# Kernel optimization log

Hardware: AMD Instinct MI355X
Metric: run time of the kernel (lower is better)

## Reference

```python
import jax, jax.numpy as jnp
import numpy as np

B, T, D_IN = 4096, 1024, 2
EMD, CELL, D_OUT = 128, 128, 5


def setup_inputs() -> dict:
    key = jax.random.key(0)
    ks = jax.random.split(key, 9)
    s = lambda k, shape, fan: jax.random.normal(k, shape, jnp.float32) / np.sqrt(fan)
    return {
        "inputs": jax.random.normal(ks[0], (B, T, D_IN), jnp.float32),
        "We": s(ks[1], (EMD, D_IN), D_IN),
        "be": s(ks[2], (EMD,), D_IN),
        "W_ih": s(ks[3], (4 * CELL, EMD), EMD),
        "W_hh": s(ks[4], (4 * CELL, CELL), CELL),
        "b_ih": s(ks[5], (4 * CELL,), CELL),
        "b_hh": s(ks[6], (4 * CELL,), CELL),
        "Wo": s(ks[7], (D_OUT, CELL), CELL),
        "bo": s(ks[8], (D_OUT,), CELL),
    }


def reference(inputs, We, be, W_ih, W_hh, b_ih, b_hh, Wo, bo):
    """VanillaLSTM forward: per-step embed MLP -> LSTMCell -> output MLP.
    inputs: [B, T, D_IN]; returns (outputs [B, T, D_OUT], h [B,CELL], c [B,CELL])."""
    Bsz = inputs.shape[0]
    cell = W_hh.shape[1]

    def step(hc, x_t):
        h, c = hc
        # input embedding MLP (Linear + ReLU, batch_norm=False)
        e = jax.nn.relu(x_t @ We.T + be)                      # [B, EMD]
        # torch.nn.LSTMCell gate math
        gates = e @ W_ih.T + b_ih + h @ W_hh.T + b_hh         # [B, 4*CELL]
        i, f, g, o = jnp.split(gates, 4, axis=-1)
        i, f, o = jax.nn.sigmoid(i), jax.nn.sigmoid(f), jax.nn.sigmoid(o)
        g = jnp.tanh(g)
        c_new = f * c + i * g
        h_new = o * jnp.tanh(c_new)
        # output embedding (Linear, no activation)
        y = h_new @ Wo.T + bo                                 # [B, D_OUT]
        return (h_new, c_new), y

    h0 = jnp.zeros((Bsz, cell), inputs.dtype)
    c0 = jnp.zeros((Bsz, cell), inputs.dtype)
    xs = jnp.swapaxes(inputs, 0, 1)                           # [T, B, D_IN]
    (h, c), ys = jax.lax.scan(step, (h0, c0), xs)
    outputs = jnp.swapaxes(ys, 0, 1)                          # [B, T, D_OUT]
    return outputs, h, c
```

## Files before the change

kernel.cpp:

```cpp
#include <hip/hip_runtime.h>
#include <hip/hip_bf16.h>


#define B_TOT 4096
#define T_LEN 1024
#define D_INP 2
#define EMD   128
#define CELL  128
#define D_OUT 5

#define ROWS  16
#define WAVES 8
#define BLOCK (WAVES * 64)
#define LDH   136

typedef short s8v  __attribute__((ext_vector_type(8)));
typedef short s4v  __attribute__((ext_vector_type(4)));
typedef float f32x4 __attribute__((ext_vector_type(4)));

#define BAR() asm volatile("s_waitcnt lgkmcnt(0)\n\ts_barrier" ::: "memory")

#if __has_builtin(__builtin_amdgcn_exp2f)
#define EXP2F(x) __builtin_amdgcn_exp2f(x)
#else
#define EXP2F(x) exp2f(x)
#endif
#if __has_builtin(__builtin_amdgcn_rcpf)
#define RCPF(x) __builtin_amdgcn_rcpf(x)
#else
#define RCPF(x) (1.0f / (x))
#endif

__device__ __forceinline__ float bf2f(short s) {
    unsigned int u = ((unsigned int)(unsigned short)s) << 16;
    return __builtin_bit_cast(float, u);
}
__device__ __forceinline__ short f2bf(float f) {
    unsigned int u = __builtin_bit_cast(unsigned int, f);
    u += 0x7fffu + ((u >> 16) & 1u);
    return (short)(u >> 16);
}
__device__ __forceinline__ unsigned int pk_bf16(float a, float b) {
    unsigned int ua = __builtin_bit_cast(unsigned int, a);
    unsigned int ub = __builtin_bit_cast(unsigned int, b);
    return ((ua + 0x8000u) >> 16) | ((ub + 0x8000u) & 0xffff0000u);
}
__device__ __forceinline__ float sigm(float x) {
    return RCPF(1.0f + EXP2F(-1.44269504f * x));
}
__device__ __forceinline__ float tanh_fast(float x) {
    return 2.0f * RCPF(1.0f + EXP2F(-2.88539008f * x)) - 1.0f;
}
__device__ __forceinline__ s8v load8_f32_to_bf16(const float* p) {
    float4 a = *(const float4*)p;
    float4 b = *(const float4*)(p + 4);
    s8v r;
    r[0] = f2bf(a.x); r[1] = f2bf(a.y); r[2] = f2bf(a.z); r[3] = f2bf(a.w);
    r[4] = f2bf(b.x); r[5] = f2bf(b.y); r[6] = f2bf(b.z); r[7] = f2bf(b.w);
    return r;
}

__global__ __launch_bounds__(BLOCK, 1)
void lstm_persistent(const float* __restrict__ x,
                     const float* __restrict__ We,
                     const float* __restrict__ be,
                     const float* __restrict__ Wih,
                     const float* __restrict__ Whh,
                     const float* __restrict__ bih,
                     const float* __restrict__ bhh,
                     const float* __restrict__ Wo,
                     const float* __restrict__ bo,
                     float* __restrict__ out)
{
    __shared__ short h_lds[2][ROWS][LDH];
    __shared__ short e_lds[2][ROWS][LDH];

    const int tid  = threadIdx.x;
    const int lane = tid & 63;
    const int w    = tid >> 6;
    const int n16  = lane & 15;
    const int q    = lane >> 4;
    const int q8   = q * 8;
    const int b0   = blockIdx.x * ROWS;
    const int ch0  = w * 16 + q * 4;

    float* out_y = out;
    float* out_h = out + (size_t)B_TOT * T_LEN * D_OUT;
    float* out_c = out_h + (size_t)B_TOT * CELL;

    s8v wih_f[4][4], whh_f[4][4];
    #pragma unroll
    for (int g = 0; g < 4; ++g) {
        const int row = g * CELL + w * 16 + n16;
        #pragma unroll
        for (int kt = 0; kt < 4; ++kt) {
            wih_f[g][kt] = load8_f32_to_bf16(Wih + row * EMD  + kt * 32 + q8);
            whh_f[g][kt] = load8_f32_to_bf16(Whh + row * CELL + kt * 32 + q8);
        }
    }
    float4 bias4[4];
    #pragma unroll
    for (int g = 0; g < 4; ++g) {
        float4 bi = *(const float4*)(bih + g * CELL + ch0);
        float4 bh = *(const float4*)(bhh + g * CELL + ch0);
        bias4[g] = make_float4(bi.x + bh.x, bi.y + bh.y, bi.z + bh.z, bi.w + bh.w);
    }

    s8v wo_f[4];
    float bo_r[4];
    {
        s8v z = {0, 0, 0, 0, 0, 0, 0, 0};
        #pragma unroll
        for (int kt = 0; kt < 4; ++kt) wo_f[kt] = z;
        if (w == 0 && n16 < D_OUT) {
            #pragma unroll
            for (int kt = 0; kt < 4; ++kt)
                wo_f[kt] = load8_f32_to_bf16(Wo + n16 * CELL + kt * 32 + q8);
        }
        #pragma unroll
        for (int r = 0; r < 4; ++r) {
            const int oc = q * 4 + r;
            bo_r[r] = (w == 0 && oc < D_OUT) ? bo[oc] : 0.0f;
        }
    }

    const int er  = tid >> 5;
    const int jj0 = (tid & 31) * 4;
    float weA[4], weB[4], bev[4];
    #pragma unroll
    for (int jl = 0; jl < 4; ++jl) {
        weA[jl] = We[(jj0 + jl) * 2 + 0];
        weB[jl] = We[(jj0 + jl) * 2 + 1];
        bev[jl] = be[jj0 + jl];
    }
    const float* xrow = x + (size_t)(b0 + er) * T_LEN * D_INP;

    {
        unsigned int* hz = (unsigned int*)&h_lds[0][0][0];
        for (int i = tid; i < ROWS * LDH / 2; i += BLOCK) hz[i] = 0u;

        float2 xd = *(const float2*)(xrow);
        float e0 = fmaxf(xd.x * weA[0] + xd.y * weB[0] + bev[0], 0.0f);
        float e1 = fmaxf(xd.x * weA[1] + xd.y * weB[1] + bev[1], 0.0f);
        float e2 = fmaxf(xd.x * weA[2] + xd.y * weB[2] + bev[2], 0.0f);
        float e3 = fmaxf(xd.x * weA[3] + xd.y * weB[3] + bev[3], 0.0f);
        unsigned int u01 = pk_bf16(e0, e1), u23 = pk_bf16(e2, e3);
        *(unsigned int*)&e_lds[0][er][jj0]     = u01;
        *(unsigned int*)&e_lds[0][er][jj0 + 2] = u23;
    }

    float c_r[4] = {0.0f, 0.0f, 0.0f, 0.0f};

    #pragma unroll 1
    for (int u = 0; u < T_LEN; ++u) {
        const int p = u & 1;
        BAR();

        const int tn = (u + 1 < T_LEN) ? (u + 1) : (T_LEN - 1);
        float2 xd = *(const float2*)(xrow + tn * D_INP);

        s8v ah[4], ae[4];
        #pragma unroll
        for (int kt = 0; kt < 4; ++kt) {
            ah[kt] = *(const s8v*)&h_lds[p][n16][kt * 32 + q8];
            ae[kt] = *(const s8v*)&e_lds[p][n16][kt * 32 + q8];
        }

        if (w == 0 && u > 0) {
            f32x4 ay = {bo_r[0], bo_r[1], bo_r[2], bo_r[3]};
            #pragma unroll
            for (int kt = 0; kt < 4; ++kt)
                ay = __builtin_amdgcn_mfma_f32_16x16x32_bf16(wo_f[kt], ah[kt], ay, 0, 0, 0);
            float* yp = out_y + ((size_t)(b0 + n16) * T_LEN + (u - 1)) * D_OUT;
            if (q == 0) {
                yp[0] = ay[0]; yp[1] = ay[1]; yp[2] = ay[2]; yp[3] = ay[3];
            } else if (q == 1) {
                yp[4] = ay[0];
            }
        }

        f32x4 acc[4];
        #pragma unroll
        for (int g = 0; g < 4; ++g) {
            f32x4 a = {bias4[g].x, bias4[g].y, bias4[g].z, bias4[g].w};
            #pragma unroll
            for (int kt = 0; kt < 4; ++kt) {
                a = __builtin_amdgcn_mfma_f32_16x16x32_bf16(whh_f[g][kt], ah[kt], a, 0, 0, 0);
                a = __builtin_amdgcn_mfma_f32_16x16x32_bf16(wih_f[g][kt], ae[kt], a, 0, 0, 0);
            }
            acc[g] = a;
        }

        float hv[4];
        #pragma unroll
        for (int r = 0; r < 4; ++r) {
            float iv = sigm(acc[0][r]);
            float fv = sigm(acc[1][r]);
            float gv = tanh_fast(acc[2][r]);
            float ov = sigm(acc[3][r]);
            c_r[r] = fv * c_r[r] + iv * gv;
            hv[r] = ov * tanh_fast(c_r[r]);
        }
        {
            unsigned int u01 = pk_bf16(hv[0], hv[1]);
            unsigned int u23 = pk_bf16(hv[2], hv[3]);
            unsigned int* hp = (unsigned int*)&h_lds[1 - p][n16][ch0];
            hp[0] = u01; hp[1] = u23;
        }
        if (u == T_LEN - 1) {
            *(float4*)(out_h + (size_t)(b0 + n16) * CELL + ch0) =
                make_float4(hv[0], hv[1], hv[2], hv[3]);
        }

        {
            float e0 = fmaxf(xd.x * weA[0] + xd.y * weB[0] + bev[0], 0.0f);
            float e1 = fmaxf(xd.x * weA[1] + xd.y * weB[1] + bev[1], 0.0f);
            float e2 = fmaxf(xd.x * weA[2] + xd.y * weB[2] + bev[2], 0.0f);
            float e3 = fmaxf(xd.x * weA[3] + xd.y * weB[3] + bev[3], 0.0f);
            unsigned int u01 = pk_bf16(e0, e1), u23 = pk_bf16(e2, e3);
            unsigned int* ep = (unsigned int*)&e_lds[1 - p][er][jj0];
            ep[0] = u01; ep[1] = u23;
        }
    }

    BAR();

    if (w == 0) {
        s8v ah[4];
        #pragma unroll
        for (int kt = 0; kt < 4; ++kt)
            ah[kt] = *(const s8v*)&h_lds[0][n16][kt * 32 + q8];
        f32x4 ay = {bo_r[0], bo_r[1], bo_r[2], bo_r[3]};
        #pragma unroll
        for (int kt = 0; kt < 4; ++kt)
            ay = __builtin_amdgcn_mfma_f32_16x16x32_bf16(wo_f[kt], ah[kt], ay, 0, 0, 0);
        float* yp = out_y + ((size_t)(b0 + n16) * T_LEN + (T_LEN - 1)) * D_OUT;
        if (q == 0) {
            yp[0] = ay[0]; yp[1] = ay[1]; yp[2] = ay[2]; yp[3] = ay[3];
        } else if (q == 1) {
            yp[4] = ay[0];
        }
    }

    *(float4*)(out_c + (size_t)(b0 + n16) * CELL + ch0) =
        make_float4(c_r[0], c_r[1], c_r[2], c_r[3]);
}

extern "C" void kernel_launch(void* const* d_in, const int* in_sizes, int n_in,
                              void* d_out, int out_size, void* d_ws, size_t ws_size,
                              hipStream_t stream) {
    const float* x   = (const float*)d_in[0];
    const float* We  = (const float*)d_in[1];
    const float* be  = (const float*)d_in[2];
    const float* Wih = (const float*)d_in[3];
    const float* Whh = (const float*)d_in[4];
    const float* bih = (const float*)d_in[5];
    const float* bhh = (const float*)d_in[6];
    const float* Wo  = (const float*)d_in[7];
    const float* bo  = (const float*)d_in[8];
    float* out = (float*)d_out;

    dim3 grid(B_TOT / ROWS);
    dim3 block(BLOCK);
    hipLaunchKernelGGL(lstm_persistent, grid, block, 0, stream,
                       x, We, be, Wih, Whh, bih, bhh, Wo, bo, out);
}
```

Measured before the change: 1.394 ms.

## Prescale gate weights by exp2 constants, split MFMA chains, unroll timestep loop by two

The weights and biases are multiplied by -log2(e), or by -2·log2(e) for the g gate, before conversion to bf16. This removes the per-element multiply inside the sigmoid and tanh gate activations. The single dependent chain of 8 MFMAs per gate becomes two independent 4-MFMA chains (input and hidden) summed afterwards, which shortens the MFMA dependency latency. The time loop is also unrolled by two with compile-time ping-pong buffer indices, so LDS addresses are constant. Rounding the prescaled weights to bf16 changes numerics slightly.

```diff
diff --git a/kernel.cpp b/kernel.cpp
--- a/kernel.cpp
+++ b/kernel.cpp
@@ -1,5 +1,6 @@
 #include <hip/hip_runtime.h>
 #include <hip/hip_bf16.h>
+#include <type_traits>
 
 
 #define B_TOT 4096
@@ -15,7 +16,6 @@
 #define LDH   136
 
 typedef short s8v  __attribute__((ext_vector_type(8)));
-typedef short s4v  __attribute__((ext_vector_type(4)));
 typedef float f32x4 __attribute__((ext_vector_type(4)));
 
 #define BAR() asm volatile("s_waitcnt lgkmcnt(0)\n\ts_barrier" ::: "memory")
@@ -31,10 +31,6 @@
 #define RCPF(x) (1.0f / (x))
 #endif
 
-__device__ __forceinline__ float bf2f(short s) {
-    unsigned int u = ((unsigned int)(unsigned short)s) << 16;
-    return __builtin_bit_cast(float, u);
-}
 __device__ __forceinline__ short f2bf(float f) {
     unsigned int u = __builtin_bit_cast(unsigned int, f);
     u += 0x7fffu + ((u >> 16) & 1u);
@@ -45,18 +41,15 @@
     unsigned int ub = __builtin_bit_cast(unsigned int, b);
     return ((ua + 0x8000u) >> 16) | ((ub + 0x8000u) & 0xffff0000u);
 }
-__device__ __forceinline__ float sigm(float x) {
-    return RCPF(1.0f + EXP2F(-1.44269504f * x));
-}
 __device__ __forceinline__ float tanh_fast(float x) {
     return 2.0f * RCPF(1.0f + EXP2F(-2.88539008f * x)) - 1.0f;
 }
-__device__ __forceinline__ s8v load8_f32_to_bf16(const float* p) {
+__device__ __forceinline__ s8v load8_scaled(const float* p, float s) {
     float4 a = *(const float4*)p;
     float4 b = *(const float4*)(p + 4);
     s8v r;
-    r[0] = f2bf(a.x); r[1] = f2bf(a.y); r[2] = f2bf(a.z); r[3] = f2bf(a.w);
-    r[4] = f2bf(b.x); r[5] = f2bf(b.y); r[6] = f2bf(b.z); r[7] = f2bf(b.w);
+    r[0] = f2bf(a.x * s); r[1] = f2bf(a.y * s); r[2] = f2bf(a.z * s); r[3] = f2bf(a.w * s);
+    r[4] = f2bf(b.x * s); r[5] = f2bf(b.y * s); r[6] = f2bf(b.z * s); r[7] = f2bf(b.w * s);
     return r;
 }
 
@@ -88,14 +81,16 @@
     float* out_h = out + (size_t)B_TOT * T_LEN * D_OUT;
     float* out_c = out_h + (size_t)B_TOT * CELL;
 
+    const float GSC[4] = {-1.44269504f, -1.44269504f, -2.88539008f, -1.44269504f};
+
     s8v wih_f[4][4], whh_f[4][4];
     #pragma unroll
     for (int g = 0; g < 4; ++g) {
         const int row = g * CELL + w * 16 + n16;
         #pragma unroll
         for (int kt = 0; kt < 4; ++kt) {
-            wih_f[g][kt] = load8_f32_to_bf16(Wih + row * EMD  + kt * 32 + q8);
-            whh_f[g][kt] = load8_f32_to_bf16(Whh + row * CELL + kt * 32 + q8);
+            wih_f[g][kt] = load8_scaled(Wih + row * EMD  + kt * 32 + q8, GSC[g]);
+            whh_f[g][kt] = load8_scaled(Whh + row * CELL + kt * 32 + q8, GSC[g]);
         }
     }
     float4 bias4[4];
@@ -103,7 +98,8 @@
     for (int g = 0; g < 4; ++g) {
         float4 bi = *(const float4*)(bih + g * CELL + ch0);
         float4 bh = *(const float4*)(bhh + g * CELL + ch0);
-        bias4[g] = make_float4(bi.x + bh.x, bi.y + bh.y, bi.z + bh.z, bi.w + bh.w);
+        bias4[g] = make_float4((bi.x + bh.x) * GSC[g], (bi.y + bh.y) * GSC[g],
+                               (bi.z + bh.z) * GSC[g], (bi.w + bh.w) * GSC[g]);
     }
 
     s8v wo_f[4];
@@ -115,7 +111,7 @@
         if (w == 0 && n16 < D_OUT) {
             #pragma unroll
             for (int kt = 0; kt < 4; ++kt)
-                wo_f[kt] = load8_f32_to_bf16(Wo + n16 * CELL + kt * 32 + q8);
+                wo_f[kt] = load8_scaled(Wo + n16 * CELL + kt * 32 + q8, 1.0f);
         }
         #pragma unroll
         for (int r = 0; r < 4; ++r) {
@@ -144,16 +140,14 @@
         float e1 = fmaxf(xd.x * weA[1] + xd.y * weB[1] + bev[1], 0.0f);
         float e2 = fmaxf(xd.x * weA[2] + xd.y * weB[2] + bev[2], 0.0f);
         float e3 = fmaxf(xd.x * weA[3] + xd.y * weB[3] + bev[3], 0.0f);
-        unsigned int u01 = pk_bf16(e0, e1), u23 = pk_bf16(e2, e3);
-        *(unsigned int*)&e_lds[0][er][jj0]     = u01;
-        *(unsigned int*)&e_lds[0][er][jj0 + 2] = u23;
+        unsigned int* ep = (unsigned int*)&e_lds[0][er][jj0];
+        ep[0] = pk_bf16(e0, e1); ep[1] = pk_bf16(e2, e3);
     }
 
     float c_r[4] = {0.0f, 0.0f, 0.0f, 0.0f};
 
-    #pragma unroll 1
-    for (int u = 0; u < T_LEN; ++u) {
-        const int p = u & 1;
+    auto step = [&](int u, auto Pc) {
+        constexpr int P = decltype(Pc)::value;
         BAR();
 
         const int tn = (u + 1 < T_LEN) ? (u + 1) : (T_LEN - 1);
@@ -162,8 +156,21 @@
         s8v ah[4], ae[4];
         #pragma unroll
         for (int kt = 0; kt < 4; ++kt) {
-            ah[kt] = *(const s8v*)&h_lds[p][n16][kt * 32 + q8];
-            ae[kt] = *(const s8v*)&e_lds[p][n16][kt * 32 + q8];
+            ah[kt] = *(const s8v*)&h_lds[P][n16][kt * 32 + q8];
+            ae[kt] = *(const s8v*)&e_lds[P][n16][kt * 32 + q8];
+        }
+
+        f32x4 acc_e[4], acc_h[4];
+        #pragma unroll
+        for (int g = 0; g < 4; ++g) {
+            f32x4 a = {bias4[g].x, bias4[g].y, bias4[g].z, bias4[g].w};
+            f32x4 b = {0.0f, 0.0f, 0.0f, 0.0f};
+            #pragma unroll
+            for (int kt = 0; kt < 4; ++kt) {
+                a = __builtin_amdgcn_mfma_f32_16x16x32_bf16(wih_f[g][kt], ae[kt], a, 0, 0, 0);
+                b = __builtin_amdgcn_mfma_f32_16x16x32_bf16(whh_f[g][kt], ah[kt], b, 0, 0, 0);
+            }
+            acc_e[g] = a; acc_h[g] = b;
         }
 
         if (w == 0 && u > 0) {
@@ -172,55 +179,46 @@
             for (int kt = 0; kt < 4; ++kt)
                 ay = __builtin_amdgcn_mfma_f32_16x16x32_bf16(wo_f[kt], ah[kt], ay, 0, 0, 0);
             float* yp = out_y + ((size_t)(b0 + n16) * T_LEN + (u - 1)) * D_OUT;
-            if (q == 0) {
-                yp[0] = ay[0]; yp[1] = ay[1]; yp[2] = ay[2]; yp[3] = ay[3];
-            } else if (q == 1) {
-                yp[4] = ay[0];
-            }
-        }
-
-        f32x4 acc[4];
-        #pragma unroll
-        for (int g = 0; g < 4; ++g) {
-            f32x4 a = {bias4[g].x, bias4[g].y, bias4[g].z, bias4[g].w};
-            #pragma unroll
-            for (int kt = 0; kt < 4; ++kt) {
-                a = __builtin_amdgcn_mfma_f32_16x16x32_bf16(whh_f[g][kt], ah[kt], a, 0, 0, 0);
-                a = __builtin_amdgcn_mfma_f32_16x16x32_bf16(wih_f[g][kt], ae[kt], a, 0, 0, 0);
-            }
-            acc[g] = a;
+            if (q == 0) { yp[0] = ay[0]; yp[1] = ay[1]; yp[2] = ay[2]; yp[3] = ay[3]; }
+            else if (q == 1) { yp[4] = ay[0]; }
         }
 
         float hv[4];
         #pragma unroll
         for (int r = 0; r < 4; ++r) {
-            float iv = sigm(acc[0][r]);
-            float fv = sigm(acc[1][r]);
-            float gv = tanh_fast(acc[2][r]);
-            float ov = sigm(acc[3][r]);
+            float si = acc_e[0][r] + acc_h[0][r];
+            float sf = acc_e[1][r] + acc_h[1][r];
+            float sg = acc_e[2][r] + acc_h[2][r];
+            float so = acc_e[3][r] + acc_h[3][r];
+            float iv = RCPF(1.0f + EXP2F(si));
+            float fv = RCPF(1.0f + EXP2F(sf));
+            float gv = 2.0f * RCPF(1.0f + EXP2F(sg)) - 1.0f;
+            float ov = RCPF(1.0f + EXP2F(so));
             c_r[r] = fv * c_r[r] + iv * gv;
             hv[r] = ov * tanh_fast(c_r[r]);
         }
         {
-            unsigned int u01 = pk_bf16(hv[0], hv[1]);
-            unsigned int u23 = pk_bf16(hv[2], hv[3]);
-            unsigned int* hp = (unsigned int*)&h_lds[1 - p][n16][ch0];
-            hp[0] = u01; hp[1] = u23;
+            unsigned int* hp = (unsigned int*)&h_lds[1 - P][n16][ch0];
+            hp[0] = pk_bf16(hv[0], hv[1]); hp[1] = pk_bf16(hv[2], hv[3]);
         }
         if (u == T_LEN - 1) {
             *(float4*)(out_h + (size_t)(b0 + n16) * CELL + ch0) =
                 make_float4(hv[0], hv[1], hv[2], hv[3]);
         }
-
         {
             float e0 = fmaxf(xd.x * weA[0] + xd.y * weB[0] + bev[0], 0.0f);
             float e1 = fmaxf(xd.x * weA[1] + xd.y * weB[1] + bev[1], 0.0f);
             float e2 = fmaxf(xd.x * weA[2] + xd.y * weB[2] + bev[2], 0.0f);
             float e3 = fmaxf(xd.x * weA[3] + xd.y * weB[3] + bev[3], 0.0f);
-            unsigned int u01 = pk_bf16(e0, e1), u23 = pk_bf16(e2, e3);
-            unsigned int* ep = (unsigned int*)&e_lds[1 - p][er][jj0];
-            ep[0] = u01; ep[1] = u23;
-        }
+            unsigned int* ep = (unsigned int*)&e_lds[1 - P][er][jj0];
+            ep[0] = pk_bf16(e0, e1); ep[1] = pk_bf16(e2, e3);
+        }
+    };
+
+    #pragma unroll 1
+    for (int u = 0; u < T_LEN; u += 2) {
+        step(u,     std::integral_constant<int, 0>{});
+        step(u + 1, std::integral_constant<int, 1>{});
     }
 
     BAR();
```

New measurement: 1.320 ms. 1.06x faster.
